# Optimization experiments

Hardware: AMD Instinct MI355X
Metric: run time of the kernel (lower is better)

The kernel has to match this reference:

```python
import jax, jax.numpy as jnp
import numpy as np

NUM_EMBEDDINGS = 1024
EMBEDDING_DIM = 128
COMMITMENT_COST = 0.25


def setup_inputs() -> dict:
    key = jax.random.key(0)
    k_in, k_cb = jax.random.split(key)
    inputs = jax.random.normal(k_in, (8, EMBEDDING_DIM, 16, 32, 32), dtype=jnp.float32)
    # torch init: uniform_(-1/num_embeddings, 1/num_embeddings)
    codebook = jax.random.uniform(
        k_cb, (NUM_EMBEDDINGS, EMBEDDING_DIM), dtype=jnp.float32,
        minval=-1.0 / NUM_EMBEDDINGS, maxval=1.0 / NUM_EMBEDDINGS)
    return {"inputs": inputs, "codebook": codebook}


def reference(inputs, codebook):
    # inputs: [B, C, D, H, W] with C == embedding_dim; codebook: [K, C]
    C = codebook.shape[1]
    flat = jnp.transpose(inputs, (0, 2, 3, 4, 1)).reshape(-1, C)  # [N, C]
    # squared L2 distances via the expanded form (matches torch code)
    distances = (jnp.sum(flat ** 2, axis=1, keepdims=True)
                 + jnp.sum(codebook ** 2, axis=1)
                 - 2.0 * flat @ codebook.T)  # [N, K]
    encoding_indices = jnp.argmin(distances, axis=1)  # [N]
    quantized = codebook[encoding_indices]  # [N, C]
    # NOTE: faithful to original bug — plain reshape back to channels-first
    # inputs.shape with no inverse permute (torch: quantized.view(inputs.shape))
    quantized = quantized.reshape(inputs.shape)
    e_latent_loss = jnp.mean((jax.lax.stop_gradient(quantized) - inputs) ** 2)
    q_latent_loss = jnp.mean((quantized - jax.lax.stop_gradient(inputs)) ** 2)
    loss = q_latent_loss + COMMITMENT_COST * e_latent_loss
    # straight-through estimator
    quantized_st = inputs + jax.lax.stop_gradient(quantized - inputs)
    return quantized_st, loss, encoding_indices
```

## Files before the change

kernel.cpp:

```cpp
#include <hip/hip_runtime.h>

typedef unsigned short u16;
typedef __attribute__((ext_vector_type(8))) short bf16x8;
typedef __attribute__((ext_vector_type(4))) float f32x4;

#define K_CB  1024
#define N_ROWS 131072
#define NUMEL (N_ROWS * 128)
#define TAU2 6.0e-4f
#define SMALLCAP 32768
#define FULLCAP  32768

#define GLOAD16(gp, lp) __builtin_amdgcn_global_load_lds( \
    (const __attribute__((address_space(1))) unsigned int*)(gp), \
    (__attribute__((address_space(3))) unsigned int*)(lp), 16, 0, 0)

__device__ __forceinline__ u16 f2bf(float x) {
    union { float f; unsigned int u; } a; a.f = x;
    unsigned int r = a.u + 0x7fffu + ((a.u >> 16) & 1u);
    return (u16)(r >> 16);
}

__global__ void prep_cb_kernel(const float* __restrict__ cb, float* __restrict__ bn,
                               u16* __restrict__ Bpl, int* __restrict__ cnts) {
    int k = blockIdx.x * 256 + threadIdx.x;
    if (blockIdx.x == 0 && threadIdx.x < 2) cnts[threadIdx.x] = 0;
    if (k >= K_CB) return;
    const float4* row4 = reinterpret_cast<const float4*>(cb) + k * 32;
    float s = 0.f;
    #pragma unroll
    for (int i = 0; i < 32; ++i) {
        float4 v = row4[i];
        s = fmaf(v.x, v.x, s); s = fmaf(v.y, v.y, s);
        s = fmaf(v.z, v.z, s); s = fmaf(v.w, v.w, s);
    }
    bn[k] = s;
    const float* rf = cb + k * 128;
    #pragma unroll
    for (int s8 = 0; s8 < 16; ++s8) {
        unsigned int hw[8];
        #pragma unroll
        for (int j = 0; j < 8; ++j) hw[j] = f2bf(rf[s8 * 8 + j]);
        uint4 H;
        H.x = hw[0] | (hw[1] << 16); H.y = hw[2] | (hw[3] << 16);
        H.z = hw[4] | (hw[5] << 16); H.w = hw[6] | (hw[7] << 16);
        *reinterpret_cast<uint4*>(&Bpl[((size_t)s8 * 1024 + k) * 8]) = H;
    }
}

__launch_bounds__(256, 3)
__global__ void gemm_fused_kernel(const float* __restrict__ in, const float* __restrict__ cb,
                                  const u16* __restrict__ Bpl, const float* __restrict__ bn,
                                  float* __restrict__ out_q, float* __restrict__ idx_out,
                                  uint2* __restrict__ smallL, int* __restrict__ fullL,
                                  int* __restrict__ cnts,
                                  float* __restrict__ deltas, float* __restrict__ partials) {
    __shared__ u16 A_s[16 * 64 * 8];
    __shared__ u16 Bb[2 * 4 * 256 * 8];
    __shared__ float bn_s[K_CB];
    __shared__ float red_s[4];

    const int tid = threadIdx.x;
    const int w = tid >> 6, lane = tid & 63, g4 = lane >> 4, l15 = lane & 15;
    const int blk = blockIdx.x, n0 = blk * 64;

    #pragma unroll
    for (int i = 0; i < 4; ++i) {
        const u16* g = Bpl + (size_t)(w * 1024 + i * 64 + lane) * 8;
        GLOAD16(g, &Bb[(w * 256 + i * 64) * 8]);
    }
    for (int i = tid; i < K_CB; i += 256) bn_s[i] = bn[i];

    {
        const int base = (n0 >> 14) * (128 * 16384) + (n0 & 16383);
        #pragma unroll 1
        for (int i = 0; i < 4; ++i) {
            int p = tid + i * 256;
            int n = p & 63, s = p >> 6;
            const float* g = in + base + (size_t)(s * 8) * 16384 + n;
            unsigned int pw[8];
            #pragma unroll
            for (int j = 0; j < 8; ++j) pw[j] = f2bf(g[(size_t)j * 16384]);
            uint4 H;
            H.x = pw[0] | (pw[1] << 16); H.y = pw[2] | (pw[3] << 16);
            H.z = pw[4] | (pw[5] << 16); H.w = pw[6] | (pw[7] << 16);
            *reinterpret_cast<uint4*>(&A_s[(s * 64 + n) * 8]) = H;
        }
    }
    __syncthreads();

    f32x4 acc[4][4];
    const f32x4 zz = {0.f, 0.f, 0.f, 0.f};
    #pragma unroll
    for (int mi = 0; mi < 4; ++mi)
        #pragma unroll
        for (int ni = 0; ni < 4; ++ni) acc[mi][ni] = zz;

    float b1[16], b2[16]; int i1[16];
    #pragma unroll
    for (int sl = 0; sl < 16; ++sl) { b1[sl] = 3.4e38f; b2[sl] = 3.4e38f; i1[sl] = 0; }

    #pragma unroll 1
    for (int t = 0; t < 16; ++t) {
        const int chunk = t >> 2, cc = t & 3, buf = t & 1;
        if (t < 15) {
            const int t2 = t + 1, chunk2 = t2 >> 2, cc2 = t2 & 3, nb = t2 & 1;
            #pragma unroll
            for (int i = 0; i < 4; ++i) {
                const u16* g = Bpl + (size_t)((cc2 * 4 + w) * 1024 + chunk2 * 256 + i * 64 + lane) * 8;
                GLOAD16(g, &Bb[((nb * 4 + w) * 256 + i * 64) * 8]);
            }
            asm volatile("s_waitcnt vmcnt(4)" ::: "memory");
        } else {
            asm volatile("s_waitcnt vmcnt(0)" ::: "memory");
        }
        __builtin_amdgcn_s_barrier();

        bf16x8 af[4], bfr[4];
        #pragma unroll
        for (int mi = 0; mi < 4; ++mi)
            af[mi] = *reinterpret_cast<const bf16x8*>(
                &A_s[((cc * 4 + g4) * 64 + mi * 16 + l15) * 8]);
        #pragma unroll
        for (int ni = 0; ni < 4; ++ni)
            bfr[ni] = *reinterpret_cast<const bf16x8*>(
                &Bb[((buf * 4 + g4) * 256 + w * 64 + ni * 16 + l15) * 8]);
        #pragma unroll
        for (int mi = 0; mi < 4; ++mi)
            #pragma unroll
            for (int ni = 0; ni < 4; ++ni)
                acc[mi][ni] = __builtin_amdgcn_mfma_f32_16x16x32_bf16(
                    af[mi], bfr[ni], acc[mi][ni], 0, 0, 0);

        if (cc == 3) {
            #pragma unroll
            for (int ni = 0; ni < 4; ++ni) {
                int n = chunk * 256 + w * 64 + ni * 16 + l15;
                float bnv = bn_s[n];
                #pragma unroll
                for (int mi = 0; mi < 4; ++mi) {
                    #pragma unroll
                    for (int r = 0; r < 4; ++r) {
                        float s = fmaf(-2.0f, acc[mi][ni][r], bnv);
                        int sl = mi * 4 + r;
                        if (s < b1[sl]) { b2[sl] = b1[sl]; b1[sl] = s; i1[sl] = n; }
                        else if (s < b2[sl]) b2[sl] = s;
                    }
                    acc[mi][ni] = zz;
                }
            }
        }
        asm volatile("s_waitcnt lgkmcnt(0)" ::: "memory");
        __builtin_amdgcn_s_barrier();
    }

    float* m_b1   = (float*)Bb;
    float* m_b2   = m_b1 + 256;
    int*   m_i1   = (int*)(m_b2 + 256);
    int*   idx_s  = m_i1 + 256;
    float* gmin_s = (float*)(idx_s + 64);
    int*   flg_s  = (int*)(gmin_s + 64);
    int*   ccnt_s = flg_s + 64;
    int*   fb_s   = ccnt_s + 64;
    int*   cand_s = fb_s + 64;
    uint2* sRec_s = (uint2*)(cand_s + 256);
    int*   fRow_s = (int*)(sRec_s + 64);
    int*   aux_s  = fRow_s + 64;

    #pragma unroll
    for (int sl = 0; sl < 16; ++sl) {
        float v1 = b1[sl], v2 = b2[sl]; int ix = i1[sl];
        #pragma unroll
        for (int m = 1; m < 16; m <<= 1) {
            float o1 = __shfl_xor(v1, m, 64);
            int   oi = __shfl_xor(ix, m, 64);
            float o2 = __shfl_xor(v2, m, 64);
            if (o1 < v1 || (o1 == v1 && oi < ix)) { v2 = fminf(v1, o2); v1 = o1; ix = oi; }
            else v2 = fminf(v2, o1);
        }
        if (l15 == 0) {
            int mi = sl >> 2, r = sl & 3;
            int rl = mi * 16 + g4 * 4 + r;
            m_b1[w * 64 + rl] = v1; m_b2[w * 64 + rl] = v2; m_i1[w * 64 + rl] = ix;
        }
    }
    __syncthreads();
    if (tid < 64) {
        float v1 = m_b1[tid], v2 = m_b2[tid]; int ix = m_i1[tid];
        #pragma unroll
        for (int wv = 1; wv < 4; ++wv) {
            float o1 = m_b1[wv * 64 + tid], o2 = m_b2[wv * 64 + tid]; int oi = m_i1[wv * 64 + tid];
            if (o1 < v1 || (o1 == v1 && oi < ix)) { v2 = fminf(v1, o2); v1 = o1; ix = oi; }
            else v2 = fminf(v2, o1);
        }
        idx_s[tid] = ix;
        idx_out[n0 + tid] = (float)ix;
        deltas[n0 + tid] = 0.f;
        gmin_s[tid] = v1;
        flg_s[tid] = (v2 - v1 <= TAU2) ? 1 : 0;
        ccnt_s[tid] = 0;
        fb_s[tid] = 0;
        if (tid < 2) aux_s[tid] = 0;
    }
    __syncthreads();

    #pragma unroll
    for (int sl = 0; sl < 16; ++sl) {
        int mi = sl >> 2, r = sl & 3;
        int rl = mi * 16 + g4 * 4 + r;
        if (flg_s[rl]) {
            float g = gmin_s[rl];
            if (b1[sl] - g <= TAU2) {
                int p = atomicAdd(&ccnt_s[rl], 1);
                if (p < 4) cand_s[rl * 4 + p] = i1[sl]; else fb_s[rl] = 1;
            }
            if (b2[sl] - g <= TAU2) fb_s[rl] = 1;
        }
    }
    __syncthreads();

    if (tid < 64 && flg_s[tid]) {
        int nc = ccnt_s[tid];
        int row = n0 + tid;
        if (!fb_s[tid] && nc >= 2) {
            unsigned long long key = (unsigned long long)row |
                                     ((unsigned long long)nc << 20);
            for (int j = 0; j < nc; ++j)
                key |= (unsigned long long)(cand_s[tid * 4 + j] & 1023) << (24 + 10 * j);
            int p = atomicAdd(&aux_s[0], 1);
            uint2 rec; rec.x = (unsigned)key; rec.y = (unsigned)(key >> 32);
            sRec_s[p] = rec;
        } else if (fb_s[tid]) {
            int q = atomicAdd(&aux_s[1], 1);
            fRow_s[q] = row;
        }
    }
    __syncthreads();
    if (tid == 0)  aux_s[2] = (aux_s[0] > 0) ? atomicAdd(&cnts[0], aux_s[0]) : 0;
    if (tid == 64) aux_s[3] = (aux_s[1] > 0) ? atomicAdd(&cnts[1], aux_s[1]) : 0;
    __syncthreads();
    if (tid < aux_s[0]) {
        int p = aux_s[2] + tid;
        if (p < SMALLCAP) smallL[p] = sRec_s[tid];
        else {
            int q = atomicAdd(&cnts[1], 1);
            if (q < FULLCAP) fullL[q] = (int)(sRec_s[tid].x & 131071u);
        }
    }
    if (tid >= 64 && tid < 128 && (tid - 64) < aux_s[1]) {
        int p = aux_s[3] + (tid - 64);
        if (p < FULLCAP) fullL[p] = fRow_s[tid - 64];
    }
    __syncthreads();

    float acc_l = 0.f;
    const float4* cb4 = reinterpret_cast<const float4*>(cb);
    const float4* in4 = reinterpret_cast<const float4*>(in);
    float4* out4 = reinterpret_cast<float4*>(out_q);
    #pragma unroll 1
    for (int i = 0; i < 8; ++i) {
        int idx = tid + i * 256;
        int row = idx >> 5;
        int c4 = idx & 31;
        int kq = idx_s[row];
        float4 q = cb4[kq * 32 + c4];
        float4 x = in4[(size_t)(n0 + row) * 32 + c4];
        float4 d, o;
        d.x = q.x - x.x; d.y = q.y - x.y; d.z = q.z - x.z; d.w = q.w - x.w;
        o.x = x.x + d.x; o.y = x.y + d.y; o.z = x.z + d.z; o.w = x.w + d.w;
        out4[(size_t)(n0 + row) * 32 + c4] = o;
        acc_l += d.x * d.x; acc_l += d.y * d.y; acc_l += d.z * d.z; acc_l += d.w * d.w;
    }
    #pragma unroll
    for (int m = 1; m < 64; m <<= 1) acc_l += __shfl_xor(acc_l, m, 64);
    if (lane == 0) red_s[w] = acc_l;
    __syncthreads();
    if (tid == 0) partials[blk] = red_s[0] + red_s[1] + red_s[2] + red_s[3];
}

__device__ __forceinline__ void patch_row(const float* __restrict__ in,
                                          const float* __restrict__ cb,
                                          float* __restrict__ idx_out,
                                          float* __restrict__ out_q,
                                          float* __restrict__ deltas,
                                          int row, int k_new, int lane) {
    int k_old = (int)idx_out[row];
    if (k_new == k_old) return;
    if (lane == 0) idx_out[row] = (float)k_new;
    float dd = 0.f;
    if (lane < 32) {
        const float4* in4 = reinterpret_cast<const float4*>(in);
        const float4* cb4 = reinterpret_cast<const float4*>(cb);
        float4* out4 = reinterpret_cast<float4*>(out_q);
        float4 x = in4[(size_t)row * 32 + lane];
        float4 qn = cb4[(size_t)k_new * 32 + lane];
        float4 qo = cb4[(size_t)k_old * 32 + lane];
        float4 dn, dl, o;
        dn.x = qn.x - x.x; dn.y = qn.y - x.y; dn.z = qn.z - x.z; dn.w = qn.w - x.w;
        o.x = x.x + dn.x; o.y = x.y + dn.y; o.z = x.z + dn.z; o.w = x.w + dn.w;
        out4[(size_t)row * 32 + lane] = o;
        dl.x = qo.x - x.x; dl.y = qo.y - x.y; dl.z = qo.z - x.z; dl.w = qo.w - x.w;
        dd = dn.x * dn.x + dn.y * dn.y + dn.z * dn.z + dn.w * dn.w
           - (dl.x * dl.x + dl.y * dl.y + dl.z * dl.z + dl.w * dl.w);
    }
    #pragma unroll
    for (int m = 1; m < 64; m <<= 1) dd += __shfl_xor(dd, m, 64);
    if (lane == 0) deltas[row] = dd;
}

__global__ void small_rescore_kernel(const float* __restrict__ in, const float* __restrict__ cb,
                                     const float* __restrict__ bn, const uint2* __restrict__ recs,
                                     const int* __restrict__ cnts, float* __restrict__ idx_out,
                                     float* __restrict__ out_q, float* __restrict__ deltas) {
    __shared__ float xls[4][128];
    const int tid = threadIdx.x, wv = tid >> 6, lane = tid & 63;
    int ns = cnts[0]; if (ns > SMALLCAP) ns = SMALLCAP;
    float* xl = xls[wv];
    for (int f = blockIdx.x * 4 + wv; f < ns; f += gridDim.x * 4) {
        uint2 rc = recs[f];
        unsigned long long key = ((unsigned long long)rc.y << 32) | (unsigned long long)rc.x;
        int row = (int)(key & 131071ull);
        int nc = (int)((key >> 20) & 7ull);
        int ck = (lane < 4) ? (int)((key >> (24 + 10 * lane)) & 1023ull) : 0;
        const float* bp = in + (size_t)(row >> 14) * 2097152 + (row & 16383);
        xl[2 * lane]     = bp[(size_t)(2 * lane) * 16384];
        xl[2 * lane + 1] = bp[(size_t)(2 * lane + 1) * 16384];
        asm volatile("s_waitcnt vmcnt(0) lgkmcnt(0)" ::: "memory");
        float xn = 0.f;
        for (int c = 0; c < 128; ++c) { float v = xl[c]; xn = fmaf(v, v, xn); }
        float s = 3.4e38f; int kk = 0x7fffffff;
        if (lane < nc) {
            const float4* cr = reinterpret_cast<const float4*>(cb + (size_t)ck * 128);
            float dot = 0.f;
            #pragma unroll
            for (int c4 = 0; c4 < 32; ++c4) {
                float4 bv = cr[c4];
                float4 xv = *reinterpret_cast<const float4*>(&xl[c4 * 4]);
                dot = fmaf(xv.x, bv.x, dot); dot = fmaf(xv.y, bv.y, dot);
                dot = fmaf(xv.z, bv.z, dot); dot = fmaf(xv.w, bv.w, dot);
            }
            float t1 = xn + bn[ck];
            s = fmaf(-2.0f, dot, t1);
            kk = ck;
        }
        #pragma unroll
        for (int m = 1; m < 4; m <<= 1) {
            float os = __shfl_xor(s, m, 64);
            int ok = __shfl_xor(kk, m, 64);
            if (os < s || (os == s && ok < kk)) { s = os; kk = ok; }
        }
        int k_new = __shfl(kk, 0, 64);
        patch_row(in, cb, idx_out, out_q, deltas, row, k_new, lane);
    }
}

__global__ void full_rescore_kernel(const float* __restrict__ in, const float* __restrict__ cb,
                                    const float* __restrict__ bn, const int* __restrict__ fullL,
                                    const int* __restrict__ cnts, float* __restrict__ idx_out,
                                    float* __restrict__ out_q, float* __restrict__ deltas) {
    __shared__ float xls[4][128];
    const int tid = threadIdx.x, wv = tid >> 6, lane = tid & 63;
    int nf = cnts[1]; if (nf > FULLCAP) nf = FULLCAP;
    float* xl = xls[wv];
    for (int f = blockIdx.x * 4 + wv; f < nf; f += gridDim.x * 4) {
        int row = fullL[f];
        const float* bp = in + (size_t)(row >> 14) * 2097152 + (row & 16383);
        xl[2 * lane]     = bp[(size_t)(2 * lane) * 16384];
        xl[2 * lane + 1] = bp[(size_t)(2 * lane + 1) * 16384];
        asm volatile("s_waitcnt vmcnt(0) lgkmcnt(0)" ::: "memory");
        float xn = 0.f;
        for (int c = 0; c < 128; ++c) { float v = xl[c]; xn = fmaf(v, v, xn); }
        float best = 3.4e38f; int bi = 0x7fffffff;
        for (int j = 0; j < 16; ++j) {
            int k = j * 64 + lane;
            const float4* cr = reinterpret_cast<const float4*>(cb + (size_t)k * 128);
            float dot = 0.f;
            #pragma unroll
            for (int c4 = 0; c4 < 32; ++c4) {
                float4 bv = cr[c4];
                float4 xv = *reinterpret_cast<const float4*>(&xl[c4 * 4]);
                dot = fmaf(xv.x, bv.x, dot); dot = fmaf(xv.y, bv.y, dot);
                dot = fmaf(xv.z, bv.z, dot); dot = fmaf(xv.w, bv.w, dot);
            }
            float t1 = xn + bn[k];
            float s = fmaf(-2.0f, dot, t1);
            if (s < best || (s == best && k < bi)) { best = s; bi = k; }
        }
        #pragma unroll
        for (int m = 1; m < 64; m <<= 1) {
            float os = __shfl_xor(best, m, 64);
            int ok = __shfl_xor(bi, m, 64);
            if (os < best || (os == best && ok < bi)) { best = os; bi = ok; }
        }
        int k_new = __shfl(bi, 0, 64);
        patch_row(in, cb, idx_out, out_q, deltas, row, k_new, lane);
    }
}

__global__ void loss_stage1(const float* __restrict__ partials, const float* __restrict__ deltas,
                            float* __restrict__ part2) {
    __shared__ float red_s[4];
    const int blk = blockIdx.x, tid = threadIdx.x;
    float s = 0.f;
    const float* dp = deltas + blk * 2048;
    for (int i = tid; i < 2048; i += 256) s += dp[i];
    if (tid < 32) s += partials[blk * 32 + tid];
    #pragma unroll
    for (int m = 1; m < 64; m <<= 1) s += __shfl_xor(s, m, 64);
    if ((tid & 63) == 0) red_s[tid >> 6] = s;
    __syncthreads();
    if (tid == 0) part2[blk] = red_s[0] + red_s[1] + red_s[2] + red_s[3];
}

__global__ void loss_stage2(const float* __restrict__ part2, float* __restrict__ out_loss) {
    const int tid = threadIdx.x;
    float s = part2[tid];
    #pragma unroll
    for (int m = 1; m < 64; m <<= 1) s += __shfl_xor(s, m, 64);
    if (tid == 0) out_loss[0] = 1.25f * (s / (float)NUMEL);
}

extern "C" void kernel_launch(void* const* d_in, const int* in_sizes, int n_in,
                              void* d_out, int out_size, void* d_ws, size_t ws_size,
                              hipStream_t stream) {
    (void)in_sizes; (void)n_in; (void)out_size; (void)ws_size;
    const float* in = (const float*)d_in[0];
    const float* cb = (const float*)d_in[1];
    float* out = (float*)d_out;

    char* ws = (char*)d_ws;
    float* bn       = (float*)(ws + 0);
    u16*   Bpl      = (u16*)(ws + 4096);
    uint2* smallL   = (uint2*)(ws + 528384);
    int*   fullL    = (int*)(ws + 790528);
    float* deltas   = (float*)(ws + 921600);
    float* partials = (float*)(ws + 1445888);
    float* part2    = (float*)(ws + 1454080);
    int*   cnts     = (int*)(ws + 1454336);

    float* idxf = out + NUMEL + 1;

    prep_cb_kernel<<<4, 256, 0, stream>>>(cb, bn, Bpl, cnts);
    gemm_fused_kernel<<<2048, 256, 0, stream>>>(in, cb, Bpl, bn, out, idxf,
                                                smallL, fullL, cnts, deltas, partials);
    small_rescore_kernel<<<1024, 256, 0, stream>>>(in, cb, bn, smallL, cnts, idxf, out, deltas);
    full_rescore_kernel<<<256, 256, 0, stream>>>(in, cb, bn, fullL, cnts, idxf, out, deltas);
    loss_stage1<<<64, 256, 0, stream>>>(partials, deltas, part2);
    loss_stage2<<<1, 64, 0, stream>>>(part2, out + NUMEL);
}
```

Measured before the change: 290.0 us.

## Load codebook fragments directly to registers instead of double-buffered LDS

Drops the LDS double buffer and async global-to-LDS loads for the bf16 codebook. Each wave now loads its B fragments straight from global (L2) into registers, with a one-step register prefetch and no per-iteration barriers. The K loop now runs 32 steps of 4x2 MFMA tiles instead of 16 steps of 4x4, which halves B register reuse and moves more traffic through L2. It also lowers the grid sizes of the small and full rescore kernels.

```diff
diff --git a/kernel.cpp b/kernel.cpp
--- a/kernel.cpp
+++ b/kernel.cpp
@@ -10,10 +10,6 @@
 #define TAU2 6.0e-4f
 #define SMALLCAP 32768
 #define FULLCAP  32768
-
-#define GLOAD16(gp, lp) __builtin_amdgcn_global_load_lds( \
-    (const __attribute__((address_space(1))) unsigned int*)(gp), \
-    (__attribute__((address_space(3))) unsigned int*)(lp), 16, 0, 0)
 
 __device__ __forceinline__ u16 f2bf(float x) {
     union { float f; unsigned int u; } a; a.f = x;
@@ -56,20 +52,21 @@
                                   int* __restrict__ cnts,
                                   float* __restrict__ deltas, float* __restrict__ partials) {
     __shared__ u16 A_s[16 * 64 * 8];
-    __shared__ u16 Bb[2 * 4 * 256 * 8];
     __shared__ float bn_s[K_CB];
+    __shared__ float m_b1s[256], m_b2s[256];
+    __shared__ int   m_i1s[256];
+    __shared__ int   idx_s[64];
+    __shared__ float gmin_s[64];
+    __shared__ int   flg_s[64], ccnt_s[64], fb_s[64];
+    __shared__ int   cand_s[256];
+    __shared__ uint2 sRec_s[64];
+    __shared__ int   fRow_s[64];
+    __shared__ int   aux_s[4];
     __shared__ float red_s[4];
 
     const int tid = threadIdx.x;
     const int w = tid >> 6, lane = tid & 63, g4 = lane >> 4, l15 = lane & 15;
     const int blk = blockIdx.x, n0 = blk * 64;
-
-    #pragma unroll
-    for (int i = 0; i < 4; ++i) {
-        const u16* g = Bpl + (size_t)(w * 1024 + i * 64 + lane) * 8;
-        GLOAD16(g, &Bb[(w * 256 + i * 64) * 8]);
-    }
-    for (int i = tid; i < K_CB; i += 256) bn_s[i] = bn[i];
 
     {
         const int base = (n0 >> 14) * (128 * 16384) + (n0 & 16383);
@@ -87,55 +84,47 @@
             *reinterpret_cast<uint4*>(&A_s[(s * 64 + n) * 8]) = H;
         }
     }
-    __syncthreads();
-
-    f32x4 acc[4][4];
+    for (int i = tid; i < K_CB; i += 256) bn_s[i] = bn[i];
+    __syncthreads();
+
+    f32x4 acc[4][2];
     const f32x4 zz = {0.f, 0.f, 0.f, 0.f};
     #pragma unroll
-    for (int mi = 0; mi < 4; ++mi)
-        #pragma unroll
-        for (int ni = 0; ni < 4; ++ni) acc[mi][ni] = zz;
+    for (int mi = 0; mi < 4; ++mi) { acc[mi][0] = zz; acc[mi][1] = zz; }
 
     float b1[16], b2[16]; int i1[16];
     #pragma unroll
     for (int sl = 0; sl < 16; ++sl) { b1[sl] = 3.4e38f; b2[sl] = 3.4e38f; i1[sl] = 0; }
 
+    const u16* bbase = Bpl + (size_t)(g4 * 1024 + w * 32 + l15) * 8;
+
+    bf16x8 bc0 = *reinterpret_cast<const bf16x8*>(bbase);
+    bf16x8 bc1 = *reinterpret_cast<const bf16x8*>(bbase + 128);
+
     #pragma unroll 1
-    for (int t = 0; t < 16; ++t) {
-        const int chunk = t >> 2, cc = t & 3, buf = t & 1;
-        if (t < 15) {
-            const int t2 = t + 1, chunk2 = t2 >> 2, cc2 = t2 & 3, nb = t2 & 1;
-            #pragma unroll
-            for (int i = 0; i < 4; ++i) {
-                const u16* g = Bpl + (size_t)((cc2 * 4 + w) * 1024 + chunk2 * 256 + i * 64 + lane) * 8;
-                GLOAD16(g, &Bb[((nb * 4 + w) * 256 + i * 64) * 8]);
-            }
-            asm volatile("s_waitcnt vmcnt(4)" ::: "memory");
-        } else {
-            asm volatile("s_waitcnt vmcnt(0)" ::: "memory");
-        }
-        __builtin_amdgcn_s_barrier();
-
-        bf16x8 af[4], bfr[4];
+    for (int t = 0; t < 32; ++t) {
+        const int cc = t & 3, chunk = t >> 2;
+        bf16x8 bx0, bx1;
+        if (t < 31) {
+            const int t2 = t + 1, cc2 = t2 & 3, ch2 = t2 >> 2;
+            const u16* p = bbase + (size_t)(cc2 * 4 * 1024 + ch2 * 128) * 8;
+            bx0 = *reinterpret_cast<const bf16x8*>(p);
+            bx1 = *reinterpret_cast<const bf16x8*>(p + 128);
+        }
+        bf16x8 af[4];
         #pragma unroll
         for (int mi = 0; mi < 4; ++mi)
             af[mi] = *reinterpret_cast<const bf16x8*>(
                 &A_s[((cc * 4 + g4) * 64 + mi * 16 + l15) * 8]);
         #pragma unroll
-        for (int ni = 0; ni < 4; ++ni)
-            bfr[ni] = *reinterpret_cast<const bf16x8*>(
-                &Bb[((buf * 4 + g4) * 256 + w * 64 + ni * 16 + l15) * 8]);
-        #pragma unroll
-        for (int mi = 0; mi < 4; ++mi)
-            #pragma unroll
-            for (int ni = 0; ni < 4; ++ni)
-                acc[mi][ni] = __builtin_amdgcn_mfma_f32_16x16x32_bf16(
-                    af[mi], bfr[ni], acc[mi][ni], 0, 0, 0);
-
+        for (int mi = 0; mi < 4; ++mi) {
+            acc[mi][0] = __builtin_amdgcn_mfma_f32_16x16x32_bf16(af[mi], bc0, acc[mi][0], 0, 0, 0);
+            acc[mi][1] = __builtin_amdgcn_mfma_f32_16x16x32_bf16(af[mi], bc1, acc[mi][1], 0, 0, 0);
+        }
         if (cc == 3) {
             #pragma unroll
-            for (int ni = 0; ni < 4; ++ni) {
-                int n = chunk * 256 + w * 64 + ni * 16 + l15;
+            for (int ni = 0; ni < 2; ++ni) {
+                int n = chunk * 128 + w * 32 + ni * 16 + l15;
                 float bnv = bn_s[n];
                 #pragma unroll
                 for (int mi = 0; mi < 4; ++mi) {
@@ -150,22 +139,8 @@
                 }
             }
         }
-        asm volatile("s_waitcnt lgkmcnt(0)" ::: "memory");
-        __builtin_amdgcn_s_barrier();
-    }
-
-    float* m_b1   = (float*)Bb;
-    float* m_b2   = m_b1 + 256;
-    int*   m_i1   = (int*)(m_b2 + 256);
-    int*   idx_s  = m_i1 + 256;
-    float* gmin_s = (float*)(idx_s + 64);
-    int*   flg_s  = (int*)(gmin_s + 64);
-    int*   ccnt_s = flg_s + 64;
-    int*   fb_s   = ccnt_s + 64;
-    int*   cand_s = fb_s + 64;
-    uint2* sRec_s = (uint2*)(cand_s + 256);
-    int*   fRow_s = (int*)(sRec_s + 64);
-    int*   aux_s  = fRow_s + 64;
+        if (t < 31) { bc0 = bx0; bc1 = bx1; }
+    }
 
     #pragma unroll
     for (int sl = 0; sl < 16; ++sl) {
@@ -181,15 +156,15 @@
         if (l15 == 0) {
             int mi = sl >> 2, r = sl & 3;
             int rl = mi * 16 + g4 * 4 + r;
-            m_b1[w * 64 + rl] = v1; m_b2[w * 64 + rl] = v2; m_i1[w * 64 + rl] = ix;
+            m_b1s[w * 64 + rl] = v1; m_b2s[w * 64 + rl] = v2; m_i1s[w * 64 + rl] = ix;
         }
     }
     __syncthreads();
     if (tid < 64) {
-        float v1 = m_b1[tid], v2 = m_b2[tid]; int ix = m_i1[tid];
+        float v1 = m_b1s[tid], v2 = m_b2s[tid]; int ix = m_i1s[tid];
         #pragma unroll
         for (int wv = 1; wv < 4; ++wv) {
-            float o1 = m_b1[wv * 64 + tid], o2 = m_b2[wv * 64 + tid]; int oi = m_i1[wv * 64 + tid];
+            float o1 = m_b1s[wv * 64 + tid], o2 = m_b2s[wv * 64 + tid]; int oi = m_i1s[wv * 64 + tid];
             if (o1 < v1 || (o1 == v1 && oi < ix)) { v2 = fminf(v1, o2); v1 = o1; ix = oi; }
             else v2 = fminf(v2, o1);
         }
@@ -443,8 +418,8 @@
     prep_cb_kernel<<<4, 256, 0, stream>>>(cb, bn, Bpl, cnts);
     gemm_fused_kernel<<<2048, 256, 0, stream>>>(in, cb, Bpl, bn, out, idxf,
                                                 smallL, fullL, cnts, deltas, partials);
-    small_rescore_kernel<<<1024, 256, 0, stream>>>(in, cb, bn, smallL, cnts, idxf, out, deltas);
-    full_rescore_kernel<<<256, 256, 0, stream>>>(in, cb, bn, fullL, cnts, idxf, out, deltas);
+    small_rescore_kernel<<<256, 256, 0, stream>>>(in, cb, bn, smallL, cnts, idxf, out, deltas);
+    full_rescore_kernel<<<128, 256, 0, stream>>>(in, cb, bn, fullL, cnts, idxf, out, deltas);
     loss_stage1<<<64, 256, 0, stream>>>(partials, deltas, part2);
     loss_stage2<<<1, 64, 0, stream>>>(part2, out + NUMEL);
 }
```

Result: slower. 343.5 us (+18.5%).
